# Kernel tuning notes

Hardware: AMD Instinct MI355X
Metric: run time of the kernel (lower is better)

The kernel has to match this reference:

```python
import jax, jax.numpy as jnp
import numpy as np

BETA = 0.95
THRESH = 1.0
SLOPE = 25.0   # fast_sigmoid surrogate slope
NUM_STEPS = 25

@jax.custom_vjp
def spike_fn(x):
    # Heaviside forward, fast_sigmoid surrogate backward
    return (x > 0).astype(x.dtype)

def _spike_fwd(x):
    return spike_fn(x), x

def _spike_bwd(x, g):
    return (g / (SLOPE * jnp.abs(x) + 1.0) ** 2,)

spike_fn.defvjp(_spike_fwd, _spike_bwd)

def lif(cur, mem):
    # snntorch Leaky, reset_mechanism='subtract': reset from previous mem, detached
    reset = jax.lax.stop_gradient((mem - THRESH > 0).astype(mem.dtype))
    mem_new = BETA * mem + cur - reset * THRESH
    spk = spike_fn(mem_new - THRESH)
    return spk, mem_new

def setup_inputs() -> dict:
    key = jax.random.key(0)
    ks = jax.random.split(key, 11)
    B, NOISE = 2048, 100
    dims = [NOISE, 128, 256, 512, 1024, 784]
    inp = {"x": jax.random.normal(ks[0], (B, NOISE), jnp.float32)}
    for i in range(5):
        bound = 1.0 / np.sqrt(dims[i]).astype(np.float32)
        inp[f"W{i+1}"] = jax.random.uniform(ks[1 + 2 * i], (dims[i + 1], dims[i]), jnp.float32, -bound, bound)
        inp[f"b{i+1}"] = jax.random.uniform(ks[2 + 2 * i], (dims[i + 1],), jnp.float32, -bound, bound)
    return inp

def reference(x, W1, b1, W2, b2, W3, b3, W4, b4, W5, b5):
    layers = [(W1, b1), (W2, b2), (W3, b3), (W4, b4), (W5, b5)]
    B = x.shape[0]
    mems0 = [jnp.zeros((B, W.shape[0]), x.dtype) for W, _ in layers]

    def step(mems, _):
        h = x
        new_mems = []
        for i, (W, b) in enumerate(layers):
            cur = jax.nn.relu(h @ W.T + b)
            spk, m = lif(cur, mems[i])
            new_mems.append(m)
            h = spk
        return new_mems, (h, jnp.tanh(new_mems[-1]))

    _, (spk_rec, mem_rec) = jax.lax.scan(step, mems0, None, length=NUM_STEPS)
    return spk_rec, mem_rec  # each [25, B, 784]
```

## Files before the change

### kernel.cpp

```cpp
#include <hip/hip_runtime.h>
#include <math.h>


typedef _Float16 f16;
typedef __attribute__((ext_vector_type(8))) short short8;
typedef __attribute__((ext_vector_type(8))) _Float16 half8;
typedef __attribute__((ext_vector_type(4))) _Float16 half4;
typedef __attribute__((ext_vector_type(4))) float f32x4;

#define B_TOTAL 2048
#define LO_SCALE 2.44140625e-4f
#define ACC_SCALE 0.015625f
#define TILE_F16 8192

__global__ __launch_bounds__(256) void gemm_relu_f32_kernel(
    const float* __restrict__ h, const float* __restrict__ W,
    const float* __restrict__ bias, float* __restrict__ out, int N, int K) {
  __shared__ float As[16][64];
  __shared__ float Bs[16][64];

  const int t = threadIdx.x;
  const int tx = t & 15;
  const int ty = t >> 4;
  const int m0 = blockIdx.y * 64;
  const int n0 = blockIdx.x * 64;
  const int lr = t >> 2;
  const int lc = (t & 3) * 4;

  float acc[4][4];
#pragma unroll
  for (int i = 0; i < 4; ++i)
#pragma unroll
    for (int j = 0; j < 4; ++j) acc[i][j] = 0.0f;

  const int ktiles = (K + 15) / 16;
  for (int kt = 0; kt < ktiles; ++kt) {
    const int kbase = kt * 16;
    {
      const float* src = h + (size_t)(m0 + lr) * K + kbase + lc;
#pragma unroll
      for (int j = 0; j < 4; ++j) {
        const int kg = kbase + lc + j;
        As[lc + j][lr] = (kg < K) ? src[j] : 0.0f;
      }
    }
    {
      const int nr = n0 + lr;
      const float* src = W + (size_t)nr * K + kbase + lc;
#pragma unroll
      for (int j = 0; j < 4; ++j) {
        const int kg = kbase + lc + j;
        Bs[lc + j][lr] = (nr < N && kg < K) ? src[j] : 0.0f;
      }
    }
    __syncthreads();
#pragma unroll
    for (int k = 0; k < 16; ++k) {
      float a[4], bb[4];
#pragma unroll
      for (int i = 0; i < 4; ++i) a[i] = As[k][ty * 4 + i];
#pragma unroll
      for (int j = 0; j < 4; ++j) bb[j] = Bs[k][tx * 4 + j];
#pragma unroll
      for (int i = 0; i < 4; ++i)
#pragma unroll
        for (int j = 0; j < 4; ++j) acc[i][j] = fmaf(a[i], bb[j], acc[i][j]);
    }
    __syncthreads();
  }

#pragma unroll
  for (int i = 0; i < 4; ++i) {
    const int m = m0 + ty * 4 + i;
#pragma unroll
    for (int j = 0; j < 4; ++j) {
      const int n = n0 + tx * 4 + j;
      if (n < N) {
        float cur = acc[i][j] + bias[n];
        out[(size_t)m * N + n] = cur > 0.0f ? cur : 0.0f;
      }
    }
  }
}

__global__ __launch_bounds__(256) void split2_kernel(
    const float* __restrict__ W, f16* __restrict__ Wc, int total, int K) {
  const int idx = blockIdx.x * 256 + threadIdx.x;
  if (idx < total) {
    const int n = idx / K;
    const int k = idx - n * K;
    const float w64 = W[idx] * 64.0f;
    const f16 hi = (f16)w64;
    const float r = w64 - (float)hi;
    const f16 lo = (f16)(r * 4096.0f);
    const size_t base = (size_t)n * 2 * K + k;
    Wc[base] = hi;
    Wc[base + K] = lo;
  }
}

__global__ __launch_bounds__(256) void lif1_kernel(
    const float* __restrict__ cur1, f16* __restrict__ s1_all) {
  const int i0 = (blockIdx.x * 256 + (int)threadIdx.x) * 4;
  const float4 c = *(const float4*)(cur1 + i0);
  const float ca[4] = {c.x, c.y, c.z, c.w};
  float m[4] = {0.0f, 0.0f, 0.0f, 0.0f};
  for (int st = 0; st < 25; ++st) {
    half4 sv;
#pragma unroll
    for (int j = 0; j < 4; ++j) {
      const float mo = m[j];
      const float reset = (mo - 1.0f > 0.0f) ? 1.0f : 0.0f;
      float mn = __fmul_rn(0.95f, mo);
      mn = __fadd_rn(mn, ca[j]);
      mn = __fsub_rn(mn, reset);
      m[j] = mn;
      sv[j] = (f16)((mn - 1.0f > 0.0f) ? 1.0f : 0.0f);
    }
    *(half4*)(s1_all + (size_t)st * (B_TOTAL * 128) + i0) = sv;
  }
}

__global__ __launch_bounds__(256) void layer_kernel(
    const f16* __restrict__ A_all,
    const f16* __restrict__ Wc,
    const float* __restrict__ bias,
    f16* __restrict__ spk_out,
    float* __restrict__ sr, float* __restrict__ mr,
    int N, int K, int nbx, int mode) {
  extern __shared__ f16 Bsm[];

  const int t = threadIdx.x;
  const int lane = t & 63;
  const int w = t >> 6;
  const int wm = w >> 1;
  const int wn = w & 1;
  const int lb = blockIdx.x;
  const int m0 = (lb / nbx) * 64;
  const int n0 = (lb % nbx) * 64;
  const int lrow = t >> 3;
  const int lk = (t & 7) * 8;
  const int K2 = 2 * K;
  const int nk = K >> 6;

  float bias_r[2];
#pragma unroll
  for (int j = 0; j < 2; ++j) {
    const int n = n0 + wn * 32 + j * 16 + (lane & 15);
    bias_r[j] = (n < N) ? bias[n] : 0.0f;
  }

  f32x4 acch[2][2], accl[2][2], memr[2][2];
#pragma unroll
  for (int i = 0; i < 2; ++i)
#pragma unroll
    for (int j = 0; j < 2; ++j) memr[i][j] = 0.0f;

  auto zacc = [&]() {
#pragma unroll
    for (int i = 0; i < 2; ++i)
#pragma unroll
      for (int j = 0; j < 2; ++j) {
        acch[i][j] = 0.0f;
        accl[i][j] = 0.0f;
      }
  };

  auto stage = [&](int kt, int q) {
    f16* T = Bsm + q * TILE_F16;
#pragma unroll
    for (int i = 0; i < 2; ++i) {
      const int r = lrow + 32 * i;
      const int nr = n0 + r;
      short8 vh = {}, vl = {};
      if (nr < N) {
        const f16* src = Wc + (size_t)nr * K2 + kt * 64 + lk;
        vh = *(const short8*)(src);
        vl = *(const short8*)(src + K);
      }
      const int sw = lk ^ ((r & 7) << 3);
      *(short8*)(T + r * 64 + sw) = vh;
      *(short8*)(T + (64 + r) * 64 + sw) = vl;
    }
  };

  auto compute = [&](const f16* At, int q) {
    const f16* T = Bsm + q * TILE_F16;
#pragma unroll
    for (int ks = 0; ks < 64; ks += 32) {
      const int kb = ks + (lane >> 4) * 8;
      half8 af[2], bh[2], bl[2];
#pragma unroll
      for (int i = 0; i < 2; ++i)
        af[i] = *(const half8*)(At + (size_t)i * 16 * K + ks);
#pragma unroll
      for (int j = 0; j < 2; ++j) {
        const int rr = wn * 32 + j * 16 + (lane & 15);
        const int sw = kb ^ ((rr & 7) << 3);
        bh[j] = *(const half8*)(T + rr * 64 + sw);
        bl[j] = *(const half8*)(T + (64 + rr) * 64 + sw);
      }
#pragma unroll
      for (int i = 0; i < 2; ++i)
#pragma unroll
        for (int j = 0; j < 2; ++j) {
          acch[i][j] = __builtin_amdgcn_mfma_f32_16x16x32_f16(
              af[i], bh[j], acch[i][j], 0, 0, 0);
          accl[i][j] = __builtin_amdgcn_mfma_f32_16x16x32_f16(
              af[i], bl[j], accl[i][j], 0, 0, 0);
        }
    }
  };

  auto epilogue = [&](int st) {
    const int col = lane & 15;
    const int rbase = (lane >> 4) * 4;
#pragma unroll
    for (int i = 0; i < 2; ++i) {
#pragma unroll
      for (int r = 0; r < 4; ++r) {
        const int m = m0 + wm * 32 + i * 16 + rbase + r;
#pragma unroll
        for (int j = 0; j < 2; ++j) {
          const int n = n0 + wn * 32 + j * 16 + col;
          if (n < N) {
            const float v =
                __fadd_rn(acch[i][j][r], __fmul_rn(accl[i][j][r], LO_SCALE));
            float cur = __fadd_rn(__fmul_rn(v, ACC_SCALE), bias_r[j]);
            cur = cur > 0.0f ? cur : 0.0f;
            const float mo = memr[i][j][r];
            const float reset = (mo - 1.0f > 0.0f) ? 1.0f : 0.0f;
            float mn = __fmul_rn(0.95f, mo);
            mn = __fadd_rn(mn, cur);
            mn = __fsub_rn(mn, reset);
            memr[i][j][r] = mn;
            const float s = (mn - 1.0f > 0.0f) ? 1.0f : 0.0f;
            const size_t idx = (size_t)st * (B_TOTAL * (size_t)N) +
                               (size_t)m * N + n;
            if (mode == 1) {
              sr[idx] = s;
              mr[idx] = tanhf(mn);
            } else {
              spk_out[idx] = (f16)s;
            }
          }
        }
      }
    }
  };

  const f16* Acur = A_all + (size_t)(m0 + wm * 32 + (lane & 15)) * K +
                    ((lane >> 4) * 8);
  const size_t Astep = (size_t)B_TOTAL * K;

  if (nk <= 4) {
    for (int kt = 0; kt < nk; ++kt) stage(kt, kt);
    __syncthreads();
    for (int st = 0; st < 25; ++st) {
      zacc();
      for (int kt = 0; kt < nk; ++kt) compute(Acur + kt * 64, kt);
      epilogue(st);
      Acur += Astep;
    }
  } else {
    stage(0, 0);
    __syncthreads();
    zacc();
    int kt = 0, st = 0;
    const int total = 25 * nk;
    for (int it = 0; it < total; ++it) {
      const int ktn = (kt + 1 == nk) ? 0 : kt + 1;
      const bool do_stage = (it + 1 < total);
      short8 vh[2], vl[2];
      if (do_stage) {
#pragma unroll
        for (int i = 0; i < 2; ++i) {
          const int r = lrow + 32 * i;
          const int nr = n0 + r;
          vh[i] = {};
          vl[i] = {};
          if (nr < N) {
            const f16* src = Wc + (size_t)nr * K2 + ktn * 64 + lk;
            vh[i] = *(const short8*)(src);
            vl[i] = *(const short8*)(src + K);
          }
        }
      }
      compute(Acur + kt * 64, it & 1);
      if (do_stage) {
        f16* T = Bsm + ((it + 1) & 1) * TILE_F16;
#pragma unroll
        for (int i = 0; i < 2; ++i) {
          const int r = lrow + 32 * i;
          const int sw = lk ^ ((r & 7) << 3);
          *(short8*)(T + r * 64 + sw) = vh[i];
          *(short8*)(T + (64 + r) * 64 + sw) = vl[i];
        }
      }
      __syncthreads();
      if (++kt == nk) {
        kt = 0;
        epilogue(st);
        zacc();
        ++st;
        Acur += Astep;
      }
    }
  }
}

extern "C" void kernel_launch(void* const* d_in, const int* in_sizes, int n_in,
                              void* d_out, int out_size, void* d_ws,
                              size_t ws_size, hipStream_t stream) {
  const float* x = (const float*)d_in[0];
  const float* W[5];
  const float* bi[5];
  for (int i = 0; i < 5; ++i) {
    W[i] = (const float*)d_in[1 + 2 * i];
    bi[i] = (const float*)d_in[2 + 2 * i];
  }

  const int B = B_TOTAL;
  const int Ns[5] = {128, 256, 512, 1024, 784};
  const int Ks[5] = {100, 128, 256, 512, 1024};

  char* ws = (char*)d_ws;
  size_t off = 0;
  auto alloc = [&](size_t bytes) {
    void* p = ws + off;
    off = (off + bytes + 255) & ~(size_t)255;
    return p;
  };

  float* cur1 = (float*)alloc((size_t)B * 128 * 4);
  f16* s1 = (f16*)alloc((size_t)25 * B * 128 * 2);
  f16* s2 = (f16*)alloc((size_t)25 * B * 256 * 2);
  f16* s3 = (f16*)alloc((size_t)25 * B * 512 * 2);
  f16* s4 = (f16*)alloc((size_t)25 * B * 1024 * 2);
  f16* Wc[5];
  for (int i = 1; i < 5; ++i)
    Wc[i] = (f16*)alloc((size_t)Ns[i] * Ks[i] * 2 * 2);

  float* outF = (float*)d_out;
  float* spk_rec = outF;
  float* mem_rec = outF + (size_t)25 * B * 784;

  for (int i = 1; i < 5; ++i) {
    const int total = Ns[i] * Ks[i];
    split2_kernel<<<(total + 255) / 256, 256, 0, stream>>>(W[i], Wc[i], total,
                                                           Ks[i]);
  }

  gemm_relu_f32_kernel<<<dim3(2, B / 64), 256, 0, stream>>>(x, W[0], bi[0],
                                                            cur1, 128, 100);

  lif1_kernel<<<(B * 128) / 1024, 256, 0, stream>>>(cur1, s1);

  const size_t TB = (size_t)TILE_F16 * 2;
  layer_kernel<<<32 * 4, 256, 2 * TB, stream>>>(
      s1, Wc[1], bi[1], s2, nullptr, nullptr, 256, 128, 4, 0);
  layer_kernel<<<32 * 8, 256, 4 * TB, stream>>>(
      s2, Wc[2], bi[2], s3, nullptr, nullptr, 512, 256, 8, 0);
  layer_kernel<<<32 * 16, 256, 2 * TB, stream>>>(
      s3, Wc[3], bi[3], s4, nullptr, nullptr, 1024, 512, 16, 0);
  layer_kernel<<<32 * 13, 256, 2 * TB, stream>>>(
      s4, Wc[4], bi[4], nullptr, spk_rec, mem_rec, 784, 1024, 13, 1);
}
```

Before: 1.391 ms.

## Batch five timesteps per staged weight tile to amortize LDS loads

Restructures the layer kernel so each staged weight tile in shared memory is used for five timesteps at once, keeping five sets of accumulators in registers and running the LIF epilogue sequentially over them. This cuts weight re-staging, global weight reads and barrier count by a factor of five for layers with large K. Block index mapping also changes so consecutive blocks share the same weight columns. The cost is a large increase in accumulator registers, which may reduce occupancy or cause spills.

```diff
diff --git a/kernel.cpp b/kernel.cpp
--- a/kernel.cpp
+++ b/kernel.cpp
@@ -127,7 +127,7 @@
     const float* __restrict__ bias,
     f16* __restrict__ spk_out,
     float* __restrict__ sr, float* __restrict__ mr,
-    int N, int K, int nbx, int mode) {
+    int N, int K, int mode) {
   extern __shared__ f16 Bsm[];
 
   const int t = threadIdx.x;
@@ -136,8 +136,8 @@
   const int wm = w >> 1;
   const int wn = w & 1;
   const int lb = blockIdx.x;
-  const int m0 = (lb / nbx) * 64;
-  const int n0 = (lb % nbx) * 64;
+  const int m0 = (lb & 31) * 64;
+  const int n0 = (lb >> 5) * 64;
   const int lrow = t >> 3;
   const int lk = (t & 7) * 8;
   const int K2 = 2 * K;
@@ -150,7 +150,7 @@
     bias_r[j] = (n < N) ? bias[n] : 0.0f;
   }
 
-  f32x4 acch[2][2], accl[2][2], memr[2][2];
+  f32x4 acch[5][2][2], accl[5][2][2], memr[2][2];
 #pragma unroll
   for (int i = 0; i < 2; ++i)
 #pragma unroll
@@ -158,13 +158,17 @@
 
   auto zacc = [&]() {
 #pragma unroll
-    for (int i = 0; i < 2; ++i)
-#pragma unroll
-      for (int j = 0; j < 2; ++j) {
-        acch[i][j] = 0.0f;
-        accl[i][j] = 0.0f;
-      }
-  };
+    for (int s = 0; s < 5; ++s)
+#pragma unroll
+      for (int i = 0; i < 2; ++i)
+#pragma unroll
+        for (int j = 0; j < 2; ++j) {
+          acch[s][i][j] = 0.0f;
+          accl[s][i][j] = 0.0f;
+        }
+  };
+
+  const size_t Astep = (size_t)B_TOTAL * K;
 
   auto stage = [&](int kt, int q) {
     f16* T = Bsm + q * TILE_F16;
@@ -184,15 +188,12 @@
     }
   };
 
-  auto compute = [&](const f16* At, int q) {
+  auto compute_batch = [&](const f16* Abase, int q) {
     const f16* T = Bsm + q * TILE_F16;
 #pragma unroll
     for (int ks = 0; ks < 64; ks += 32) {
       const int kb = ks + (lane >> 4) * 8;
-      half8 af[2], bh[2], bl[2];
-#pragma unroll
-      for (int i = 0; i < 2; ++i)
-        af[i] = *(const half8*)(At + (size_t)i * 16 * K + ks);
+      half8 bh[2], bl[2];
 #pragma unroll
       for (int j = 0; j < 2; ++j) {
         const int rr = wn * 32 + j * 16 + (lane & 15);
@@ -201,47 +202,59 @@
         bl[j] = *(const half8*)(T + (64 + rr) * 64 + sw);
       }
 #pragma unroll
-      for (int i = 0; i < 2; ++i)
-#pragma unroll
-        for (int j = 0; j < 2; ++j) {
-          acch[i][j] = __builtin_amdgcn_mfma_f32_16x16x32_f16(
-              af[i], bh[j], acch[i][j], 0, 0, 0);
-          accl[i][j] = __builtin_amdgcn_mfma_f32_16x16x32_f16(
-              af[i], bl[j], accl[i][j], 0, 0, 0);
-        }
-    }
-  };
-
-  auto epilogue = [&](int st) {
+      for (int s = 0; s < 5; ++s) {
+        half8 af[2];
+#pragma unroll
+        for (int i = 0; i < 2; ++i)
+          af[i] = *(const half8*)(Abase + (size_t)s * Astep +
+                                  (size_t)i * 16 * K + ks);
+#pragma unroll
+        for (int i = 0; i < 2; ++i)
+#pragma unroll
+          for (int j = 0; j < 2; ++j) {
+            acch[s][i][j] = __builtin_amdgcn_mfma_f32_16x16x32_f16(
+                af[i], bh[j], acch[s][i][j], 0, 0, 0);
+            accl[s][i][j] = __builtin_amdgcn_mfma_f32_16x16x32_f16(
+                af[i], bl[j], accl[s][i][j], 0, 0, 0);
+          }
+      }
+    }
+  };
+
+  auto epilogue5 = [&](int st0) {
     const int col = lane & 15;
     const int rbase = (lane >> 4) * 4;
 #pragma unroll
-    for (int i = 0; i < 2; ++i) {
-#pragma unroll
-      for (int r = 0; r < 4; ++r) {
-        const int m = m0 + wm * 32 + i * 16 + rbase + r;
-#pragma unroll
-        for (int j = 0; j < 2; ++j) {
-          const int n = n0 + wn * 32 + j * 16 + col;
-          if (n < N) {
-            const float v =
-                __fadd_rn(acch[i][j][r], __fmul_rn(accl[i][j][r], LO_SCALE));
-            float cur = __fadd_rn(__fmul_rn(v, ACC_SCALE), bias_r[j]);
-            cur = cur > 0.0f ? cur : 0.0f;
-            const float mo = memr[i][j][r];
-            const float reset = (mo - 1.0f > 0.0f) ? 1.0f : 0.0f;
-            float mn = __fmul_rn(0.95f, mo);
-            mn = __fadd_rn(mn, cur);
-            mn = __fsub_rn(mn, reset);
-            memr[i][j][r] = mn;
-            const float s = (mn - 1.0f > 0.0f) ? 1.0f : 0.0f;
-            const size_t idx = (size_t)st * (B_TOTAL * (size_t)N) +
-                               (size_t)m * N + n;
-            if (mode == 1) {
-              sr[idx] = s;
-              mr[idx] = tanhf(mn);
-            } else {
-              spk_out[idx] = (f16)s;
+    for (int s = 0; s < 5; ++s) {
+      const int st = st0 + s;
+#pragma unroll
+      for (int i = 0; i < 2; ++i) {
+#pragma unroll
+        for (int r = 0; r < 4; ++r) {
+          const int m = m0 + wm * 32 + i * 16 + rbase + r;
+#pragma unroll
+          for (int j = 0; j < 2; ++j) {
+            const int n = n0 + wn * 32 + j * 16 + col;
+            if (n < N) {
+              const float v = __fadd_rn(acch[s][i][j][r],
+                                        __fmul_rn(accl[s][i][j][r], LO_SCALE));
+              float cur = __fadd_rn(__fmul_rn(v, ACC_SCALE), bias_r[j]);
+              cur = cur > 0.0f ? cur : 0.0f;
+              const float mo = memr[i][j][r];
+              const float reset = (mo - 1.0f > 0.0f) ? 1.0f : 0.0f;
+              float mn = __fmul_rn(0.95f, mo);
+              mn = __fadd_rn(mn, cur);
+              mn = __fsub_rn(mn, reset);
+              memr[i][j][r] = mn;
+              const float sp = (mn - 1.0f > 0.0f) ? 1.0f : 0.0f;
+              const size_t idx = (size_t)st * (B_TOTAL * (size_t)N) +
+                                 (size_t)m * N + n;
+              if (mode == 1) {
+                sr[idx] = sp;
+                mr[idx] = tanhf(mn);
+              } else {
+                spk_out[idx] = (f16)sp;
+              }
             }
           }
         }
@@ -251,23 +264,22 @@
 
   const f16* Acur = A_all + (size_t)(m0 + wm * 32 + (lane & 15)) * K +
                     ((lane >> 4) * 8);
-  const size_t Astep = (size_t)B_TOTAL * K;
 
   if (nk <= 4) {
     for (int kt = 0; kt < nk; ++kt) stage(kt, kt);
     __syncthreads();
-    for (int st = 0; st < 25; ++st) {
+    for (int b = 0; b < 5; ++b) {
       zacc();
-      for (int kt = 0; kt < nk; ++kt) compute(Acur + kt * 64, kt);
-      epilogue(st);
-      Acur += Astep;
+      for (int kt = 0; kt < nk; ++kt) compute_batch(Acur + kt * 64, kt);
+      epilogue5(b * 5);
+      Acur += 5 * Astep;
     }
   } else {
     stage(0, 0);
     __syncthreads();
     zacc();
-    int kt = 0, st = 0;
-    const int total = 25 * nk;
+    int kt = 0, st0 = 0;
+    const int total = 5 * nk;
     for (int it = 0; it < total; ++it) {
       const int ktn = (kt + 1 == nk) ? 0 : kt + 1;
       const bool do_stage = (it + 1 < total);
@@ -286,7 +298,7 @@
           }
         }
       }
-      compute(Acur + kt * 64, it & 1);
+      compute_batch(Acur + kt * 64, it & 1);
       if (do_stage) {
         f16* T = Bsm + ((it + 1) & 1) * TILE_F16;
 #pragma unroll
@@ -300,10 +312,10 @@
       __syncthreads();
       if (++kt == nk) {
         kt = 0;
-        epilogue(st);
+        epilogue5(st0);
         zacc();
-        ++st;
-        Acur += Astep;
+        st0 += 5;
+        Acur += 5 * Astep;
       }
     }
   }
@@ -358,11 +370,11 @@
 
   const size_t TB = (size_t)TILE_F16 * 2;
   layer_kernel<<<32 * 4, 256, 2 * TB, stream>>>(
-      s1, Wc[1], bi[1], s2, nullptr, nullptr, 256, 128, 4, 0);
+      s1, Wc[1], bi[1], s2, nullptr, nullptr, 256, 128, 0);
   layer_kernel<<<32 * 8, 256, 4 * TB, stream>>>(
-      s2, Wc[2], bi[2], s3, nullptr, nullptr, 512, 256, 8, 0);
+      s2, Wc[2], bi[2], s3, nullptr, nullptr, 512, 256, 0);
   layer_kernel<<<32 * 16, 256, 2 * TB, stream>>>(
-      s3, Wc[3], bi[3], s4, nullptr, nullptr, 1024, 512, 16, 0);
+      s3, Wc[3], bi[3], s4, nullptr, nullptr, 1024, 512, 0);
   layer_kernel<<<32 * 13, 256, 2 * TB, stream>>>(
-      s4, Wc[4], bi[4], nullptr, spk_rec, mem_rec, 784, 1024, 13, 1);
-}
+      s4, Wc[4], bi[4], nullptr, spk_rec, mem_rec, 784, 1024, 1);
+}
```

Result: slower. 1.566 ms (+12.5%).
